# Kernel optimization log

Measured on AMD Instinct MI355X. Metric: run time of the kernel, lower is better.

Reference implementation:

```python
import jax, jax.numpy as jnp
import numpy as np

B, N, C, H, R = 8, 1024, 768, 12, 64
HD = C // H


def setup_inputs() -> dict:
    key = jax.random.key(0)
    ks = jax.random.split(key, 16)
    def nrm(k, shape, s=0.02):
        return jax.random.normal(k, shape, jnp.float32) * s
    return {
        'x': jax.random.normal(ks[0], (B, N, C), jnp.float32),
        'Wqkv': nrm(ks[1], (3 * C, C)),
        'ssf_scale1': 1.0 + nrm(ks[2], (3 * C,)),
        'ssf_shift1': nrm(ks[3], (3 * C,)),
        'Wa': nrm(ks[4], (R, C)),            # LoRA down (sliced to sample_LoRA_dim)
        'Wb': nrm(ks[5], (3 * C, R)),        # LoRA up
        'Wrouter': nrm(ks[6], (2 * H * 3, C)),
        'brouter': nrm(ks[7], (2 * H * 3,)),
        'Wad_down': nrm(ks[8], (R, C)),      # parallel adapter down
        'bad_down': nrm(ks[9], (R,)),
        'Wad_up': nrm(ks[10], (3 * C, R)),   # parallel adapter up -> 3*dim
        'bad_up': nrm(ks[11], (3 * C,)),
        'Wproj': nrm(ks[12], (C, C)),
        'bproj': nrm(ks[13], (C,)),
        'ssf_scale2': 1.0 + nrm(ks[14], (C,)),
        'ssf_shift2': nrm(ks[15], (C,)),
    }


def reference(x, Wqkv, ssf_scale1, ssf_shift1, Wa, Wb, Wrouter, brouter,
              Wad_down, bad_down, Wad_up, bad_up, Wproj, bproj,
              ssf_scale2, ssf_shift2):
    Bx, Nx, Cx = x.shape
    scale = (Cx // H) ** -0.5

    def split_qkv(t):
        t = t.reshape(Bx, Nx, 3, H, Cx // H).transpose(2, 0, 3, 1, 4)
        return t[0], t[1], t[2]

    # base QKV with SSF scale-shift
    q, k, v = split_qkv((x @ Wqkv.T) * ssf_scale1 + ssf_shift1)
    # LoRA delta (dropout inactive at eval)
    ql, kl, vl = split_qkv((x @ Wa.T) @ Wb.T)
    # parallel adapter delta
    qp, kp, vp = split_qkv(jax.nn.gelu(x @ Wad_down.T + bad_down, approximate=False) @ Wad_up.T + bad_up)
    # router gating: sigmoid logits -> [B,N,3,H,2]
    rs = jax.nn.sigmoid(x @ Wrouter.T + brouter).reshape(Bx, Nx, 3, H, 2)
    # faithful to source: raw reshape [B,N,3,H] -> [B,N,H,3] (index-mixing), then transpose(1,2)
    rl = rs[..., 0].reshape(Bx, Nx, H, 3).transpose(0, 2, 1, 3)  # [B,H,N,3]
    rp = rs[..., 1].reshape(Bx, Nx, H, 3).transpose(0, 2, 1, 3)
    q = q + ql * rl[..., 0:1]
    k = k + kl * rl[..., 1:2] + kp * rp[..., 1:2]
    v = v + vl * rl[..., 2:3] + vp * rp[..., 2:3]
    # standard attention (prefix path disabled: prefix_dim=0)
    attn = jax.nn.softmax(jnp.einsum('bhnd,bhmd->bhnm', q, k) * scale, axis=-1)
    o = jnp.einsum('bhnm,bhmd->bhnd', attn, v).transpose(0, 2, 1, 3).reshape(Bx, Nx, Cx)
    return (o @ Wproj.T + bproj) * ssf_scale2 + ssf_shift2
```

## Files before the change

kernel.cpp:

```cpp
#include <hip/hip_runtime.h>
#include <math.h>

typedef unsigned short u16;
typedef unsigned int u32;
typedef short s16x8 __attribute__((ext_vector_type(8)));
typedef float f32x4 __attribute__((ext_vector_type(4)));
typedef float f32x16 __attribute__((ext_vector_type(16)));
typedef u16 u16x4 __attribute__((ext_vector_type(4)));

#define DEVI __device__ __forceinline__

DEVI u16 f2bf(float f) {
  unsigned u = __builtin_bit_cast(unsigned, f);
  u += 0x7fffu + ((u >> 16) & 1u);
  return (u16)(u >> 16);
}

DEVI u32 pkbf_hu(float a, float b) {
  const u32 ua = __builtin_bit_cast(u32, a) + 0x8000u;
  const u32 ub = __builtin_bit_cast(u32, b) + 0x8000u;
  return __builtin_amdgcn_perm(ub, ua, 0x07060302u);
}

DEVI f32x4 zero4() { f32x4 z; z[0]=0.f; z[1]=0.f; z[2]=0.f; z[3]=0.f; return z; }

DEVI float xor32_max(float x) { return fmaxf(x, __shfl_xor(x, 32, 64)); }
DEVI float xor32_sum(float x) { return x + __shfl_xor(x, 32, 64); }

#define MFMA16(a,b,c) __builtin_amdgcn_mfma_f32_16x16x32_bf16((a),(b),(c),0,0,0)
#define MFMA32(a,b,c) __builtin_amdgcn_mfma_f32_32x32x16_bf16((a),(b),(c),0,0,0)

#define GLD16(gp, lp) __builtin_amdgcn_global_load_lds( \
  (const __attribute__((address_space(1))) void*)(const void*)(gp), \
  (__attribute__((address_space(3))) void*)(void*)(lp), 16, 0, 0)


__global__ __launch_bounds__(256) void prep_x(const float* __restrict__ x,
                                              u16* __restrict__ Aaug) {
  const int i = blockIdx.x * 256 + threadIdx.x;
  if (i >= 8192 * 192) return;
  const int row = i / 192, c4 = (i - row * 192) * 4;
  const float4 v = *(const float4*)(x + (size_t)row * 768 + c4);
  u16x4 o; o[0]=f2bf(v.x); o[1]=f2bf(v.y); o[2]=f2bf(v.z); o[3]=f2bf(v.w);
  *(u16x4*)(Aaug + (size_t)row * 896 + c4) = o;
}

__global__ __launch_bounds__(256) void prep_w(
    const float* __restrict__ Wqkv, const float* __restrict__ s1,
    const float* __restrict__ Wb, const float* __restrict__ Wup,
    const float* __restrict__ Wa, const float* __restrict__ Wdn,
    const float* __restrict__ Wr, const float* __restrict__ Wp,
    u16* __restrict__ Baug, u16* __restrict__ Wsm, u16* __restrict__ Wpj) {
  const int i = blockIdx.x * 256 + threadIdx.x;
  const int N1 = 2304 * 896, N2 = N1 + 256 * 768, N3 = N2 + 768 * 768;
  if (i < N1) {
    const int c = i / 896, kk = i - c * 896;
    float v;
    if (kk < 768)      v = Wqkv[(size_t)c * 768 + kk] * s1[c];
    else if (kk < 832) v = Wb[(size_t)c * 64 + (kk - 768)];
    else               v = Wup[(size_t)c * 64 + (kk - 832)];
    Baug[i] = f2bf(v);
  } else if (i < N2) {
    const int j = i - N1; const int r = j / 768, kk = j - r * 768;
    float v = 0.0f;
    if (r < 64)       v = Wa[(size_t)r * 768 + kk];
    else if (r < 128) v = Wdn[(size_t)(r - 64) * 768 + kk];
    else if (r < 200) v = Wr[(size_t)(r - 128) * 768 + kk];
    Wsm[j] = f2bf(v);
  } else if (i < N3) {
    const int j = i - N2;
    Wpj[j] = f2bf(Wp[j]);
  }
}


template <int MODE>
__global__ __launch_bounds__(256)
void gemm_mfma(const u16* __restrict__ A, int lda,
               const u16* __restrict__ Bt, int ldb,
               const float* __restrict__ p0, const float* __restrict__ p1,
               const float* __restrict__ p2,
               u16* __restrict__ ob0, u16* __restrict__ ob1, u16* __restrict__ ob2,
               float* __restrict__ of0,
               const float* __restrict__ gates) {
  __shared__ __align__(16) u16 lds[2][8192];
  __shared__ float glds[2][2][128];
  const int tid = threadIdx.x;
  const int w = tid >> 6, l = tid & 63;
  const int rl = l & 15, gq = l >> 4;
  const int wrow = (w >> 1) * 64, wcol = (w & 1) * 64;
  const int br = blockIdx.x, bc = blockIdx.y;
  const int nt = (MODE == 2) ? 28 : 24;

  const int srow = l >> 2;
  const int sslot = (l & 3) ^ ((srow >> 1) & 3);
  const u16* aSrc = A + (size_t)(br * 128 + w * 32 + srow) * lda + sslot * 8;
  const u16* bSrc = Bt + (size_t)(bc * 128 + w * 32 + srow) * ldb + sslot * 8;

  int tq = 0;
  if constexpr (MODE == 2) {
    const int g = bc * 2 + (w & 1);
    tq = g / 12;
    {
      const int gsel = tid >> 7, rr = tid & 127;
      const int gg = bc * 2 + gsel;
      const int tt = gg / 12, hh = gg % 12;
      const int f = hh * 3 + tt;
      const int ridx = (f / 12) * 24 + (f % 12) * 2;
      glds[gsel][0][rr] = gates[(size_t)(br * 128 + rr) * 72 + ridx];
      glds[gsel][1][rr] = gates[(size_t)(br * 128 + rr) * 72 + ridx + 1];
    }
  }

  f32x4 acc[4][4];
#pragma unroll
  for (int i = 0; i < 4; ++i)
#pragma unroll
    for (int j = 0; j < 4; ++j) acc[i][j] = zero4();

  auto kt_of = [&](int t) {
    if constexpr (MODE == 2) return (t < 2) ? 26 + t : ((t < 4) ? 22 + t : t - 4);
    else return t;
  };
  auto stage = [&](int kt, int buf) {
    const size_t k0 = (size_t)kt * 32;
    GLD16(aSrc + k0, &lds[buf][(w * 32) * 32]);
    GLD16(aSrc + k0 + (size_t)16 * lda, &lds[buf][(w * 32 + 16) * 32]);
    GLD16(bSrc + k0, &lds[buf][4096 + (w * 32) * 32]);
    GLD16(bSrc + k0 + (size_t)16 * ldb, &lds[buf][4096 + (w * 32 + 16) * 32]);
  };

  stage(kt_of(0), 0);
  __syncthreads();

  for (int t = 0; t < nt; ++t) {
    const int buf = t & 1;
    if (t + 1 < nt) stage(kt_of(t + 1), buf ^ 1);
    const int sl = gq ^ ((rl >> 1) & 3);
    s16x8 af[4], bfv[4];
#pragma unroll
    for (int fr = 0; fr < 4; ++fr) {
      const int row = wrow + fr * 16 + rl;
      af[fr] = *(const s16x8*)&lds[buf][row * 32 + sl * 8];
    }
#pragma unroll
    for (int fc = 0; fc < 4; ++fc) {
      const int row = wcol + fc * 16 + rl;
      bfv[fc] = *(const s16x8*)&lds[buf][4096 + row * 32 + sl * 8];
    }
#pragma unroll
    for (int fr = 0; fr < 4; ++fr)
#pragma unroll
      for (int fc = 0; fc < 4; ++fc)
        acc[fr][fc] = MFMA16(af[fr], bfv[fc], acc[fr][fc]);

    if constexpr (MODE == 2) {
      if (t == 1 || t == 3) {
        const int wsel = w & 1;
        const bool ad = (t == 1);
#pragma unroll
        for (int fr = 0; fr < 4; ++fr)
#pragma unroll
          for (int r = 0; r < 4; ++r) {
            const int rloc = wrow + fr * 16 + gq * 4 + r;
            const float gl = glds[wsel][0][rloc];
            float s;
            if (ad) { const float gp = glds[wsel][1][rloc]; s = (tq > 0) ? gp / gl : 0.0f; }
            else s = gl;
#pragma unroll
            for (int fc = 0; fc < 4; ++fc) acc[fr][fc][r] *= s;
          }
      }
    }
    __syncthreads();
  }

  if constexpr (MODE == 0) {
#pragma unroll
    for (int fc = 0; fc < 4; ++fc) {
      const int col = bc * 128 + wcol + fc * 16 + rl;
#pragma unroll
      for (int fr = 0; fr < 4; ++fr)
#pragma unroll
        for (int r = 0; r < 4; ++r) {
          const int grow = br * 128 + wrow + fr * 16 + gq * 4 + r;
          const float v = acc[fr][fc][r];
          if (col < 64) {
            ob0[(size_t)grow * 896 + 768 + col] = f2bf(v);
          } else if (col < 128) {
            const float u = v + p0[col - 64];
            const float gv = 0.5f * u * (1.0f + erff(u * 0.70710678118654752f));
            ob0[(size_t)grow * 896 + 832 + (col - 64)] = f2bf(gv);
          } else if (col < 200) {
            const float z = v + p1[col - 128];
            of0[(size_t)grow * 72 + (col - 128)] = 1.0f / (1.0f + expf(-z));
          }
        }
    }
  } else if constexpr (MODE == 1) {
#pragma unroll
    for (int fc = 0; fc < 4; ++fc) {
      const int col = bc * 128 + wcol + fc * 16 + rl;
      const float bb = p0[col], sc = p1[col], sf = p2[col];
#pragma unroll
      for (int fr = 0; fr < 4; ++fr)
#pragma unroll
        for (int r = 0; r < 4; ++r) {
          const int grow = br * 128 + wrow + fr * 16 + gq * 4 + r;
          of0[(size_t)grow * 768 + col] = (acc[fr][fc][r] + bb) * sc + sf;
        }
    }
  } else {
    const int wsel = w & 1;
    const int bq = br >> 3;
    const int n0 = (br & 7) * 128;
    const int cbase = bc * 128 + wcol;
    const int hh = (cbase % 768) / 64;
    float s1v[4], buv[4];
#pragma unroll
    for (int fc = 0; fc < 4; ++fc) {
      const int col = cbase + fc * 16 + rl;
      s1v[fc] = p0[col];
      buv[fc] = (tq > 0) ? p1[col] : 0.0f;
    }
    if (tq < 2) {
      u16* L = (u16*)&lds[0][0] + (size_t)w * 4096;
      u16* dst = (tq == 0) ? ob0 : ob1;
      const float osc = (tq == 0) ? 0.125f : 1.0f;
#pragma unroll
      for (int fr = 0; fr < 4; ++fr)
#pragma unroll
        for (int r = 0; r < 4; ++r) {
          const int nloc = fr * 16 + gq * 4 + r;
          const float gp = glds[wsel][1][wrow + nloc];
#pragma unroll
          for (int fc = 0; fc < 4; ++fc) {
            const int d = fc * 16 + rl;
            const float v = (acc[fr][fc][r] + s1v[fc] + gp * buv[fc]) * osc;
            L[nloc * 64 + (d ^ (gq << 4))] = f2bf(v);
          }
        }
      const size_t rowbase = (size_t)(bq * 12 + hh) * 1024 + n0 + wrow;
#pragma unroll
      for (int it = 0; it < 8; ++it) {
        const int nloc = it * 8 + (l >> 3);
        const int sl8 = l & 7;
        const s16x8 val =
            *(const s16x8*)&L[nloc * 64 + ((sl8 * 8) ^ (((nloc >> 2) & 3) << 4))];
        *(s16x8*)(dst + (rowbase + nloc) * 64 + sl8 * 8) = val;
      }
    } else {
      u16* L = (u16*)&lds[0][0] + (size_t)w * 4096;
#pragma unroll
      for (int fr = 0; fr < 4; ++fr)
#pragma unroll
        for (int r = 0; r < 4; ++r) {
          const int rloc = wrow + fr * 16 + gq * 4 + r;
          const float gp = glds[wsel][1][rloc];
          const int nloc = fr * 16 + gq * 4 + r;
#pragma unroll
          for (int fc = 0; fc < 4; ++fc) {
            const int d = fc * 16 + rl;
            const float v = acc[fr][fc][r] + s1v[fc] + gp * buv[fc];
            L[(d * 64 + nloc) ^ ((d & 7) << 3)] = f2bf(v);
          }
        }
      const int nw = n0 + wrow;
#pragma unroll
      for (int it = 0; it < 8; ++it) {
        const int d = it * 8 + (l >> 3);
        const int slot = l & 7;
        const s16x8 val = *(const s16x8*)&L[d * 64 + ((slot ^ (d & 7)) << 3)];
        *(s16x8*)(ob2 + ((size_t)(bq * 12 + hh) * 64 + d) * 1024 + nw + slot * 8) = val;
      }
    }
  }
}


__global__ __launch_bounds__(256)
void attn2_kernel(const u16* __restrict__ Q, const u16* __restrict__ K,
                  const u16* __restrict__ VT, u16* __restrict__ AO) {
  __shared__ __align__(16) u16 kv[2][8192];
  const int tid = threadIdx.x, w = tid >> 6, l = tid & 63;
  const int l31 = l & 31, hi = l >> 5;
  const int bh = blockIdx.x % 96, qt = blockIdx.x / 96;
  const size_t kb = (size_t)bh * (1024 * 64);
  const float LOG2E = 1.4426950408889634f;
  const float THR = 5.545177f;

  const int q0 = qt * 128 + w * 32;
  s16x8 qf[4];
  {
    const u16* qp = Q + kb + (size_t)(q0 + l31) * 64 + hi * 8;
#pragma unroll
    for (int ks = 0; ks < 4; ++ks) qf[ks] = *(const s16x8*)(qp + ks * 16);
  }

  const int srow = l >> 3;
  const int sslot = (l & 7) ^ srow;
  const u16* kSrc = K + kb + (size_t)(w * 16 + srow) * 64 + sslot * 8;
  const u16* vSrc = VT + kb + (size_t)(w * 16 + srow) * 1024 + sslot * 8;
  auto stage = [&](int t, int buf) {
    const int kv0 = t * 64;
    GLD16(kSrc + (size_t)kv0 * 64, &kv[buf][(w * 16) * 64]);
    GLD16(kSrc + (size_t)kv0 * 64 + 8 * 64, &kv[buf][(w * 16 + 8) * 64]);
    GLD16(vSrc + kv0, &kv[buf][4096 + (w * 16) * 64]);
    GLD16(vSrc + kv0 + 8 * 1024, &kv[buf][4096 + (w * 16 + 8) * 64]);
  };

  f32x16 o0, o1;
#pragma unroll
  for (int r = 0; r < 16; ++r) { o0[r] = 0.f; o1[r] = 0.f; }
  float m = -1.0e30f, lsum = 0.f;

  const int swz = l31 & 7;

  stage(0, 0);

  for (int t = 0; t < 16; ++t) {
    const int buf = t & 1;
    if (t < 15) {
      stage(t + 1, buf ^ 1);
      asm volatile("s_waitcnt vmcnt(4)" ::: "memory");
    } else {
      asm volatile("s_waitcnt vmcnt(0)" ::: "memory");
    }
    __builtin_amdgcn_s_barrier();

    f32x16 sA, sB;
#pragma unroll
    for (int r = 0; r < 16; ++r) { sA[r] = 0.f; sB[r] = 0.f; }
#pragma unroll
    for (int ks = 0; ks < 4; ++ks) {
      const int slot = (ks * 2 + hi) ^ swz;
      const s16x8 k0 = *(const s16x8*)&kv[buf][l31 * 64 + slot * 8];
      const s16x8 k1 = *(const s16x8*)&kv[buf][(32 + l31) * 64 + slot * 8];
      sA = MFMA32(k0, qf[ks], sA);
      sB = MFMA32(k1, qf[ks], sB);
    }

    float pm = sA[0];
#pragma unroll
    for (int r = 1; r < 16; ++r) pm = fmaxf(pm, sA[r]);
#pragma unroll
    for (int r = 0; r < 16; ++r) pm = fmaxf(pm, sB[r]);
    pm = xor32_max(pm);

    const bool need = pm > m + THR;
    if (__any(need)) {
      const float mnew = need ? pm : m;
      const float corr = __builtin_amdgcn_exp2f((m - mnew) * LOG2E);
      m = mnew;
      lsum *= corr;
#pragma unroll
      for (int r = 0; r < 16; ++r) {
        const int qrow = (r & 3) + 8 * (r >> 2) + 4 * hi;
        const float cr = __shfl(corr, qrow, 64);
        o0[r] *= cr; o1[r] *= cr;
      }
    }

    const float mL = m * LOG2E;
    float ps = 0.f;
#pragma unroll
    for (int r = 0; r < 16; ++r) {
      const float p = __builtin_amdgcn_exp2f(__builtin_fmaf(sA[r], LOG2E, -mL));
      sA[r] = p; ps += p;
    }
#pragma unroll
    for (int r = 0; r < 16; ++r) {
      const float p = __builtin_amdgcn_exp2f(__builtin_fmaf(sB[r], LOG2E, -mL));
      sB[r] = p; ps += p;
    }
    lsum += xor32_sum(ps);

    s16x8 pf[4];
#pragma unroll
    for (int s = 0; s < 4; ++s) {
      const f32x16 P = (s < 2) ? sA : sB;
      const int b = 8 * (s & 1);
      const u32 A0 = pkbf_hu(P[b + 0], P[b + 1]);
      const u32 A1 = pkbf_hu(P[b + 2], P[b + 3]);
      const u32 A2 = pkbf_hu(P[b + 4], P[b + 5]);
      const u32 A3 = pkbf_hu(P[b + 6], P[b + 7]);
      const u32 B0 = (u32)__shfl_xor((int)A0, 32, 64);
      const u32 B1 = (u32)__shfl_xor((int)A1, 32, 64);
      const u32 B2 = (u32)__shfl_xor((int)A2, 32, 64);
      const u32 B3 = (u32)__shfl_xor((int)A3, 32, 64);
      union { u32 u[4]; s16x8 v; } pk;
      pk.u[0] = hi ? B2 : A0;
      pk.u[1] = hi ? B3 : A1;
      pk.u[2] = hi ? A2 : B0;
      pk.u[3] = hi ? A3 : B1;
      pf[s] = pk.v;
    }

#pragma unroll
    for (int s = 0; s < 4; ++s) {
      const int slot = (s * 2 + hi) ^ swz;
      const s16x8 v0 = *(const s16x8*)&kv[buf][4096 + l31 * 64 + slot * 8];
      const s16x8 v1 = *(const s16x8*)&kv[buf][4096 + (32 + l31) * 64 + slot * 8];
      o0 = MFMA32(pf[s], v0, o0);
      o1 = MFMA32(pf[s], v1, o1);
    }
    __builtin_amdgcn_s_barrier();
  }

  const float invl = 1.0f / lsum;
  const int bq = bh / 12, h = bh % 12;
#pragma unroll
  for (int r = 0; r < 16; ++r) {
    const int qrow = (r & 3) + 8 * (r >> 2) + 4 * hi;
    const float ir = __shfl(invl, qrow, 64);
    const int n = q0 + qrow;
    u16* dst = AO + ((size_t)bq * 1024 + n) * 768 + h * 64 + l31;
    dst[0]  = f2bf(o0[r] * ir);
    dst[32] = f2bf(o1[r] * ir);
  }
}


extern "C" void kernel_launch(void* const* d_in, const int* in_sizes, int n_in,
                              void* d_out, int out_size, void* d_ws, size_t ws_size,
                              hipStream_t stream) {
  (void)in_sizes; (void)n_in; (void)out_size; (void)ws_size;
  const float* x    = (const float*)d_in[0];
  const float* Wqkv = (const float*)d_in[1];
  const float* s1   = (const float*)d_in[2];
  const float* sh1  = (const float*)d_in[3];
  const float* Wa   = (const float*)d_in[4];
  const float* Wb   = (const float*)d_in[5];
  const float* Wr   = (const float*)d_in[6];
  const float* brt  = (const float*)d_in[7];
  const float* Wdn  = (const float*)d_in[8];
  const float* bdn  = (const float*)d_in[9];
  const float* Wup  = (const float*)d_in[10];
  const float* bup  = (const float*)d_in[11];
  const float* Wp   = (const float*)d_in[12];
  const float* bpj  = (const float*)d_in[13];
  const float* sc2  = (const float*)d_in[14];
  const float* sf2  = (const float*)d_in[15];
  float* out = (float*)d_out;

  char* ws = (char*)d_ws;
  size_t off = 0;
  auto take = [&](size_t bytes) -> void* {
    void* p = ws + off;
    off = (off + bytes + 255) & ~(size_t)255;
    return p;
  };
  u16* Aaug = (u16*)take(8192UL * 896 * 2);
  u16* Baug = (u16*)take(2304UL * 896 * 2);
  u16* Wsm  = (u16*)take(256UL * 768 * 2);
  u16* Wpj  = (u16*)take(768UL * 768 * 2);
  float* gates = (float*)take(8192UL * 72 * 4);
  u16* qb  = (u16*)take(96UL * 1024 * 64 * 2);
  u16* kbf = (u16*)take(96UL * 1024 * 64 * 2);
  u16* vtb = (u16*)take(96UL * 64 * 1024 * 2);
  u16* ao  = (u16*)take(8192UL * 768 * 2);

  prep_x<<<dim3(6144), dim3(256), 0, stream>>>(x, Aaug);
  prep_w<<<dim3(11136), dim3(256), 0, stream>>>(Wqkv, s1, Wb, Wup, Wa, Wdn, Wr, Wp,
                                                Baug, Wsm, Wpj);
  gemm_mfma<0><<<dim3(64, 2), dim3(256), 0, stream>>>(
      Aaug, 896, Wsm, 768, bdn, brt, nullptr, Aaug, nullptr, nullptr, gates, nullptr);
  gemm_mfma<2><<<dim3(64, 18), dim3(256), 0, stream>>>(
      Aaug, 896, Baug, 896, sh1, bup, nullptr, qb, kbf, vtb, nullptr, gates);
  attn2_kernel<<<dim3(768), dim3(256), 0, stream>>>(qb, kbf, vtb, ao);
  gemm_mfma<1><<<dim3(64, 6), dim3(256), 0, stream>>>(
      ao, 768, Wpj, 768, bpj, sc2, sf2, nullptr, nullptr, nullptr, out, nullptr);
}
```

Measured before the change: 202.9 us.

## Triple-buffer LDS staging in GEMM and attention kernels with explicit vmcnt waits

Both the MFMA GEMM and the attention kernel move from double to triple-buffered LDS staging, prefetching two tiles ahead and waiting with explicit vmcnt counts instead of a full __syncthreads. The gate loads in the GEMM are moved after the prefetch issue, with an lgkmcnt wait. The goal is to hide more global-load latency behind MFMA work. The cost is 50% more LDS per block, which may reduce occupancy, and the correctness of the hand-counted vmcnt waits has to hold.

```diff
diff --git a/kernel.cpp b/kernel.cpp
--- a/kernel.cpp
+++ b/kernel.cpp
@@ -33,6 +33,10 @@
 #define GLD16(gp, lp) __builtin_amdgcn_global_load_lds( \
   (const __attribute__((address_space(1))) void*)(const void*)(gp), \
   (__attribute__((address_space(3))) void*)(void*)(lp), 16, 0, 0)
+
+#define WAITVM(N) asm volatile("s_waitcnt vmcnt(" #N ")" ::: "memory")
+#define WAITLG0() asm volatile("s_waitcnt lgkmcnt(0)" ::: "memory")
+#define SBAR() __builtin_amdgcn_s_barrier()
 
 
 __global__ __launch_bounds__(256) void prep_x(const float* __restrict__ x,
@@ -83,7 +87,7 @@
                u16* __restrict__ ob0, u16* __restrict__ ob1, u16* __restrict__ ob2,
                float* __restrict__ of0,
                const float* __restrict__ gates) {
-  __shared__ __align__(16) u16 lds[2][8192];
+  __shared__ __align__(16) u16 lds[3][8192];
   __shared__ float glds[2][2][128];
   const int tid = threadIdx.x;
   const int w = tid >> 6, l = tid & 63;
@@ -101,22 +105,7 @@
   if constexpr (MODE == 2) {
     const int g = bc * 2 + (w & 1);
     tq = g / 12;
-    {
-      const int gsel = tid >> 7, rr = tid & 127;
-      const int gg = bc * 2 + gsel;
-      const int tt = gg / 12, hh = gg % 12;
-      const int f = hh * 3 + tt;
-      const int ridx = (f / 12) * 24 + (f % 12) * 2;
-      glds[gsel][0][rr] = gates[(size_t)(br * 128 + rr) * 72 + ridx];
-      glds[gsel][1][rr] = gates[(size_t)(br * 128 + rr) * 72 + ridx + 1];
-    }
-  }
-
-  f32x4 acc[4][4];
-#pragma unroll
-  for (int i = 0; i < 4; ++i)
-#pragma unroll
-    for (int j = 0; j < 4; ++j) acc[i][j] = zero4();
+  }
 
   auto kt_of = [&](int t) {
     if constexpr (MODE == 2) return (t < 2) ? 26 + t : ((t < 4) ? 22 + t : t - 4);
@@ -131,11 +120,32 @@
   };
 
   stage(kt_of(0), 0);
-  __syncthreads();
+  stage(kt_of(1), 1);
+  if constexpr (MODE == 2) {
+    const int gsel = tid >> 7, rr = tid & 127;
+    const int gg = bc * 2 + gsel;
+    const int tt = gg / 12, hh = gg % 12;
+    const int f = hh * 3 + tt;
+    const int ridx = (f / 12) * 24 + (f % 12) * 2;
+    glds[gsel][0][rr] = gates[(size_t)(br * 128 + rr) * 72 + ridx];
+    glds[gsel][1][rr] = gates[(size_t)(br * 128 + rr) * 72 + ridx + 1];
+    WAITLG0();
+  }
+
+  f32x4 acc[4][4];
+#pragma unroll
+  for (int i = 0; i < 4; ++i)
+#pragma unroll
+    for (int j = 0; j < 4; ++j) acc[i][j] = zero4();
 
   for (int t = 0; t < nt; ++t) {
-    const int buf = t & 1;
-    if (t + 1 < nt) stage(kt_of(t + 1), buf ^ 1);
+    const int buf = t % 3;
+    if (t + 2 < nt) stage(kt_of(t + 2), (t + 2) % 3);
+    if (t < nt - 2)       WAITVM(8);
+    else if (t == nt - 2) WAITVM(4);
+    else                  WAITVM(0);
+    SBAR();
+
     const int sl = gq ^ ((rl >> 1) & 3);
     s16x8 af[4], bfv[4];
 #pragma unroll
@@ -172,7 +182,7 @@
           }
       }
     }
-    __syncthreads();
+    SBAR();
   }
 
   if constexpr (MODE == 0) {
@@ -281,7 +291,7 @@
 __global__ __launch_bounds__(256)
 void attn2_kernel(const u16* __restrict__ Q, const u16* __restrict__ K,
                   const u16* __restrict__ VT, u16* __restrict__ AO) {
-  __shared__ __align__(16) u16 kv[2][8192];
+  __shared__ __align__(16) u16 kv[3][8192];
   const int tid = threadIdx.x, w = tid >> 6, l = tid & 63;
   const int l31 = l & 31, hi = l >> 5;
   const int bh = blockIdx.x % 96, qt = blockIdx.x / 96;
@@ -317,16 +327,15 @@
   const int swz = l31 & 7;
 
   stage(0, 0);
+  stage(1, 1);
 
   for (int t = 0; t < 16; ++t) {
-    const int buf = t & 1;
-    if (t < 15) {
-      stage(t + 1, buf ^ 1);
-      asm volatile("s_waitcnt vmcnt(4)" ::: "memory");
-    } else {
-      asm volatile("s_waitcnt vmcnt(0)" ::: "memory");
-    }
-    __builtin_amdgcn_s_barrier();
+    const int buf = t % 3;
+    if (t + 2 < 16) stage(t + 2, (t + 2) % 3);
+    if (t < 14)       WAITVM(8);
+    else if (t == 14) WAITVM(4);
+    else              WAITVM(0);
+    SBAR();
 
     f32x16 sA, sB;
 #pragma unroll
@@ -404,7 +413,7 @@
       o0 = MFMA32(pf[s], v0, o0);
       o1 = MFMA32(pf[s], v1, o1);
     }
-    __builtin_amdgcn_s_barrier();
+    SBAR();
   }
 
   const float invl = 1.0f / lsum;
```

Result: faster. 174.2 us, median of 2 (-14.1%).
